# Performance work log

Hardware: AMD Instinct MI355X
Metric: run time of the kernel (lower is better)

Reference implementation:

```python
import jax, jax.numpy as jnp
import numpy as np

BOX = 32  # uniform ROI crop size (y1-y0 = x1-x0 = 32)


def setup_inputs() -> dict:
    key = jax.random.key(0)
    k1, k2, k3 = jax.random.split(key, 3)
    B, C, H, W = 8, 256, 200, 200
    N = 512
    feature_map = jax.random.normal(k1, (B, C, H, W), dtype=jnp.float32)
    boxes_yx = jax.random.randint(k2, (N, 2), 0, H - BOX, dtype=jnp.int32)  # top-left (y0, x0)
    assoc = jax.random.randint(k3, (N,), 0, B, dtype=jnp.int32)            # sample index per box
    return {"feature_map": feature_map, "boxes_yx": boxes_yx, "assoc": assoc}


def reference(feature_map, boxes_yx, assoc):
    # Faithful RoiCut: for each box i, crop feature_map[assoc[i], :, y0:y0+BOX, x0:x0+BOX].
    # clip_boxes=True -> clip box coords into the scene extent.
    B, C, H, W = feature_map.shape
    yx = jnp.clip(boxes_yx, 0, jnp.array([H - BOX, W - BOX], dtype=boxes_yx.dtype))

    def crop(a, yx_i):
        fm = feature_map[a]  # [C, H, W] gather of the associated sample
        return jax.lax.dynamic_slice(fm, (jnp.int32(0), yx_i[0], yx_i[1]), (C, BOX, BOX))

    box_features = jax.vmap(crop)(assoc, yx)  # [N, C, BOX, BOX]
    return box_features
```

## Files before the change

kernel.cpp:

```cpp
#include <hip/hip_runtime.h>


typedef float v4f __attribute__((ext_vector_type(4)));

constexpr int C_     = 256;
constexpr int H_     = 200;
constexpr int W_     = 200;
constexpr int BOX_   = 32;
constexpr int N_     = 512;
constexpr int B_     = 8;
constexpr int PLANE  = H_ * W_;
constexpr int HROWS  = 100;
constexpr int HLDS   = HROWS * W_;
constexpr int HLDS4  = HLDS / 4;

__global__ __launch_bounds__(512) void sort_boxes_kernel(
    const int* __restrict__ boxes,
    const int* __restrict__ assoc,
    unsigned int* __restrict__ keys,
    int* __restrict__ starts)
{
    __shared__ unsigned int key[N_];
    int t = threadIdx.x;

    int y0 = boxes[2 * t];
    int x0 = boxes[2 * t + 1];
    y0 = min(max(y0, 0), H_ - BOX_);
    x0 = min(max(x0, 0), W_ - BOX_);
    unsigned int a = (unsigned int)assoc[t];
    key[t] = (a << 25) | ((unsigned int)y0 << 17) | ((unsigned int)x0 << 9) | (unsigned int)t;
    __syncthreads();

    for (int k = 2; k <= N_; k <<= 1) {
        for (int j = k >> 1; j > 0; j >>= 1) {
            int ixj = t ^ j;
            if (ixj > t) {
                unsigned int va = key[t], vb = key[ixj];
                bool asc = ((t & k) == 0);
                if ((va > vb) == asc) { key[t] = vb; key[ixj] = va; }
            }
            __syncthreads();
        }
    }

    unsigned int v = key[t];
    keys[t] = v;
    int at = (int)(v >> 25);
    int ap = (t == 0) ? -1 : (int)(key[t - 1] >> 25);
    for (int aa = ap + 1; aa <= at; ++aa) starts[aa] = t;
    if (t == N_ - 1) for (int aa = at + 1; aa <= B_; ++aa) starts[aa] = N_;
}

__global__ __launch_bounds__(1024, 8) void roicut_kernel(
    const float* __restrict__ fm,
    const unsigned int* __restrict__ keys,
    const int* __restrict__ starts,
    float* __restrict__ out)
{
    extern __shared__ float lds[];

    int bid = blockIdx.x;
    int h = bid & 1;
    int c = (bid >> 1) & 255;
    int a = bid >> 9;
    int t = threadIdx.x;

    const v4f* src = (const v4f*)(fm + (size_t)(a * C_ + c) * PLANE) + h * HLDS4;
    v4f* l4 = (v4f*)lds;
    v4f r0 = src[t];
    v4f r1 = src[t + 1024];
    v4f r2 = src[t + 2048];
    v4f r3 = src[t + 3072];
    bool tail = t < (HLDS4 - 4096);
    v4f r4;
    if (tail) r4 = src[t + 4096];
    l4[t]        = r0;
    l4[t + 1024] = r1;
    l4[t + 2048] = r2;
    l4[t + 3072] = r3;
    if (tail) l4[t + 4096] = r4;
    __syncthreads();

    int b0 = starts[a], b1 = starts[a + 1];
    int sub = t >> 8;
    int q   = t & 255;
    int y   = q >> 3;
    int xg  = (q & 7) << 2;
    int hbase = h * HROWS;

    for (int b = b0; b < b1; b += 4) {
        int bb = b + sub;
        if (bb < b1) {
            unsigned int v = keys[bb];
            int y0 = (v >> 17) & 255;
            int x0 = (v >> 9) & 255;
            int i  = (int)(v & 511u);
            int ly = y0 + y - hbase;
            if (ly >= 0 && ly < HROWS) {
                const float* p = lds + ly * W_ + (x0 + xg);
                v4f vv;
                vv[0] = p[0];
                vv[1] = p[1];
                vv[2] = p[2];
                vv[3] = p[3];
                v4f* dst = (v4f*)(out + (((size_t)i << 18) + ((size_t)c << 10) + (size_t)(q << 2)));
                __builtin_nontemporal_store(vv, dst);
            }
        }
    }
}

extern "C" void kernel_launch(void* const* d_in, const int* in_sizes, int n_in,
                              void* d_out, int out_size, void* d_ws, size_t ws_size,
                              hipStream_t stream) {
    const float* fm    = (const float*)d_in[0];
    const int*   boxes = (const int*)d_in[1];
    const int*   assoc = (const int*)d_in[2];
    float*       out   = (float*)d_out;

    unsigned int* keys   = (unsigned int*)d_ws;
    int*          starts = (int*)d_ws + N_;

    (void)hipFuncSetAttribute((const void*)roicut_kernel,
                              hipFuncAttributeMaxDynamicSharedMemorySize,
                              HLDS * (int)sizeof(float));

    sort_boxes_kernel<<<1, N_, 0, stream>>>(boxes, assoc, keys, starts);

    int grid = B_ * C_ * 2;
    roicut_kernel<<<grid, 1024, HLDS * sizeof(float), stream>>>(fm, keys, starts, out);
}
```

Before: 172.5 us.

## Replace bitonic sort with atomic bucketing and software-pipeline the two half-plane loads

```diff
diff --git a/kernel.cpp b/kernel.cpp
--- a/kernel.cpp
+++ b/kernel.cpp
@@ -14,41 +14,36 @@
 constexpr int HLDS   = HROWS * W_;
 constexpr int HLDS4  = HLDS / 4;
 
-__global__ __launch_bounds__(512) void sort_boxes_kernel(
+__global__ __launch_bounds__(512) void group_boxes_kernel(
     const int* __restrict__ boxes,
     const int* __restrict__ assoc,
     unsigned int* __restrict__ keys,
     int* __restrict__ starts)
 {
-    __shared__ unsigned int key[N_];
+    __shared__ int cnt[B_];
+    __shared__ int base[B_ + 1];
     int t = threadIdx.x;
+
+    if (t < B_) cnt[t] = 0;
+    __syncthreads();
 
     int y0 = boxes[2 * t];
     int x0 = boxes[2 * t + 1];
     y0 = min(max(y0, 0), H_ - BOX_);
     x0 = min(max(x0, 0), W_ - BOX_);
-    unsigned int a = (unsigned int)assoc[t];
-    key[t] = (a << 25) | ((unsigned int)y0 << 17) | ((unsigned int)x0 << 9) | (unsigned int)t;
+    int a = assoc[t];
+    int pos = atomicAdd(&cnt[a], 1);
     __syncthreads();
 
-    for (int k = 2; k <= N_; k <<= 1) {
-        for (int j = k >> 1; j > 0; j >>= 1) {
-            int ixj = t ^ j;
-            if (ixj > t) {
-                unsigned int va = key[t], vb = key[ixj];
-                bool asc = ((t & k) == 0);
-                if ((va > vb) == asc) { key[t] = vb; key[ixj] = va; }
-            }
-            __syncthreads();
-        }
+    if (t == 0) {
+        int s = 0;
+        for (int i = 0; i < B_; ++i) { base[i] = s; s += cnt[i]; }
+        base[B_] = s;
     }
+    __syncthreads();
 
-    unsigned int v = key[t];
-    keys[t] = v;
-    int at = (int)(v >> 25);
-    int ap = (t == 0) ? -1 : (int)(key[t - 1] >> 25);
-    for (int aa = ap + 1; aa <= at; ++aa) starts[aa] = t;
-    if (t == N_ - 1) for (int aa = at + 1; aa <= B_; ++aa) starts[aa] = N_;
+    keys[base[a] + pos] = ((unsigned int)y0 << 17) | ((unsigned int)x0 << 9) | (unsigned int)t;
+    if (t <= B_) starts[t] = base[t];
 }
 
 __global__ __launch_bounds__(1024, 8) void roicut_kernel(
@@ -60,18 +55,24 @@
     extern __shared__ float lds[];
 
     int bid = blockIdx.x;
-    int h = bid & 1;
-    int c = (bid >> 1) & 255;
-    int a = bid >> 9;
+    int c = bid & 255;
+    int a = bid >> 8;
     int t = threadIdx.x;
 
-    const v4f* src = (const v4f*)(fm + (size_t)(a * C_ + c) * PLANE) + h * HLDS4;
+    int b0 = starts[a], b1 = starts[a + 1];
+    int sub = t >> 8;
+    int q   = t & 255;
+    int y   = q >> 3;
+    int xg  = (q & 7) << 2;
+
+    const v4f* src = (const v4f*)(fm + (size_t)(a * C_ + c) * PLANE);
     v4f* l4 = (v4f*)lds;
+    bool tail = t < (HLDS4 - 4096);
+
     v4f r0 = src[t];
     v4f r1 = src[t + 1024];
     v4f r2 = src[t + 2048];
     v4f r3 = src[t + 3072];
-    bool tail = t < (HLDS4 - 4096);
     v4f r4;
     if (tail) r4 = src[t + 4096];
     l4[t]        = r0;
@@ -81,30 +82,60 @@
     if (tail) l4[t + 4096] = r4;
     __syncthreads();
 
-    int b0 = starts[a], b1 = starts[a + 1];
-    int sub = t >> 8;
-    int q   = t & 255;
-    int y   = q >> 3;
-    int xg  = (q & 7) << 2;
-    int hbase = h * HROWS;
+    const v4f* src1 = src + HLDS4;
+    r0 = src1[t];
+    r1 = src1[t + 1024];
+    r2 = src1[t + 2048];
+    r3 = src1[t + 3072];
+    if (tail) r4 = src1[t + 4096];
+    __builtin_amdgcn_sched_barrier(0);
 
-    for (int b = b0; b < b1; b += 4) {
-        int bb = b + sub;
-        if (bb < b1) {
-            unsigned int v = keys[bb];
-            int y0 = (v >> 17) & 255;
-            int x0 = (v >> 9) & 255;
-            int i  = (int)(v & 511u);
-            int ly = y0 + y - hbase;
-            if (ly >= 0 && ly < HROWS) {
-                const float* p = lds + ly * W_ + (x0 + xg);
-                v4f vv;
-                vv[0] = p[0];
-                vv[1] = p[1];
-                vv[2] = p[2];
-                vv[3] = p[3];
-                v4f* dst = (v4f*)(out + (((size_t)i << 18) + ((size_t)c << 10) + (size_t)(q << 2)));
-                __builtin_nontemporal_store(vv, dst);
+    {
+        const int hbase = 0;
+        for (int b = b0; b < b1; b += 4) {
+            int bb = b + sub;
+            if (bb < b1) {
+                unsigned int v = keys[bb];
+                int y0 = (v >> 17) & 255;
+                int x0 = (v >> 9) & 255;
+                int i  = (int)(v & 511u);
+                int ly = y0 + y - hbase;
+                if (ly >= 0 && ly < HROWS) {
+                    const float* p = lds + ly * W_ + (x0 + xg);
+                    v4f vv;
+                    vv[0] = p[0]; vv[1] = p[1]; vv[2] = p[2]; vv[3] = p[3];
+                    v4f* dst = (v4f*)(out + (((size_t)i << 18) + ((size_t)c << 10) + (size_t)(q << 2)));
+                    __builtin_nontemporal_store(vv, dst);
+                }
+            }
+        }
+    }
+    __syncthreads();
+
+    l4[t]        = r0;
+    l4[t + 1024] = r1;
+    l4[t + 2048] = r2;
+    l4[t + 3072] = r3;
+    if (tail) l4[t + 4096] = r4;
+    __syncthreads();
+
+    {
+        const int hbase = HROWS;
+        for (int b = b0; b < b1; b += 4) {
+            int bb = b + sub;
+            if (bb < b1) {
+                unsigned int v = keys[bb];
+                int y0 = (v >> 17) & 255;
+                int x0 = (v >> 9) & 255;
+                int i  = (int)(v & 511u);
+                int ly = y0 + y - hbase;
+                if (ly >= 0 && ly < HROWS) {
+                    const float* p = lds + ly * W_ + (x0 + xg);
+                    v4f vv;
+                    vv[0] = p[0]; vv[1] = p[1]; vv[2] = p[2]; vv[3] = p[3];
+                    v4f* dst = (v4f*)(out + (((size_t)i << 18) + ((size_t)c << 10) + (size_t)(q << 2)));
+                    __builtin_nontemporal_store(vv, dst);
+                }
             }
         }
     }
@@ -125,8 +156,8 @@
                               hipFuncAttributeMaxDynamicSharedMemorySize,
                               HLDS * (int)sizeof(float));
 
-    sort_boxes_kernel<<<1, N_, 0, stream>>>(boxes, assoc, keys, starts);
+    group_boxes_kernel<<<1, N_, 0, stream>>>(boxes, assoc, keys, starts);
 
-    int grid = B_ * C_ * 2;
+    int grid = B_ * C_;
     roicut_kernel<<<grid, 1024, HLDS * sizeof(float), stream>>>(fm, keys, starts, out);
 }
```

New measurement: 176.8 us. +2.5%, slower.

## Split planes into quarter-row bands with binned box lists instead of sorted halves

Applied to the files above, without the earlier changes.

```diff
diff --git a/kernel.cpp b/kernel.cpp
--- a/kernel.cpp
+++ b/kernel.cpp
@@ -10,99 +10,107 @@
 constexpr int N_     = 512;
 constexpr int B_     = 8;
 constexpr int PLANE  = H_ * W_;
-constexpr int HROWS  = 100;
-constexpr int HLDS   = HROWS * W_;
-constexpr int HLDS4  = HLDS / 4;
+constexpr int QROWS  = 50;
+constexpr int NQ     = 4;
+constexpr int NBIN   = B_ * NQ;
+constexpr int QLDS   = QROWS * W_;
+constexpr int QLDS4  = QLDS / 4;
 
-__global__ __launch_bounds__(512) void sort_boxes_kernel(
+__global__ __launch_bounds__(512) void group_boxes_kernel(
     const int* __restrict__ boxes,
     const int* __restrict__ assoc,
     unsigned int* __restrict__ keys,
     int* __restrict__ starts)
 {
-    __shared__ unsigned int key[N_];
+    __shared__ int cnt[NBIN];
+    __shared__ int base[NBIN + 1];
     int t = threadIdx.x;
+
+    if (t < NBIN) cnt[t] = 0;
+    __syncthreads();
 
     int y0 = boxes[2 * t];
     int x0 = boxes[2 * t + 1];
     y0 = min(max(y0, 0), H_ - BOX_);
     x0 = min(max(x0, 0), W_ - BOX_);
-    unsigned int a = (unsigned int)assoc[t];
-    key[t] = (a << 25) | ((unsigned int)y0 << 17) | ((unsigned int)x0 << 9) | (unsigned int)t;
+    int a = assoc[t];
+    unsigned int key = ((unsigned int)y0 << 17) | ((unsigned int)x0 << 9) | (unsigned int)t;
+
+    int q0 = y0 / QROWS;
+    int q1 = (y0 + BOX_ - 1) / QROWS;
+    int bin0 = a * NQ + q0;
+    int p0 = atomicAdd(&cnt[bin0], 1);
+    int bin1 = -1, p1 = -1;
+    if (q1 != q0) {
+        bin1 = a * NQ + q1;
+        p1 = atomicAdd(&cnt[bin1], 1);
+    }
     __syncthreads();
 
-    for (int k = 2; k <= N_; k <<= 1) {
-        for (int j = k >> 1; j > 0; j >>= 1) {
-            int ixj = t ^ j;
-            if (ixj > t) {
-                unsigned int va = key[t], vb = key[ixj];
-                bool asc = ((t & k) == 0);
-                if ((va > vb) == asc) { key[t] = vb; key[ixj] = va; }
-            }
-            __syncthreads();
-        }
+    if (t == 0) {
+        int s = 0;
+        for (int i = 0; i < NBIN; ++i) { base[i] = s; s += cnt[i]; }
+        base[NBIN] = s;
     }
+    __syncthreads();
 
-    unsigned int v = key[t];
-    keys[t] = v;
-    int at = (int)(v >> 25);
-    int ap = (t == 0) ? -1 : (int)(key[t - 1] >> 25);
-    for (int aa = ap + 1; aa <= at; ++aa) starts[aa] = t;
-    if (t == N_ - 1) for (int aa = at + 1; aa <= B_; ++aa) starts[aa] = N_;
+    keys[base[bin0] + p0] = key;
+    if (p1 >= 0) keys[base[bin1] + p1] = key;
+    if (t <= NBIN) starts[t] = base[t];
 }
 
-__global__ __launch_bounds__(1024, 8) void roicut_kernel(
+__global__ __launch_bounds__(512, 8) void roicut_kernel(
     const float* __restrict__ fm,
     const unsigned int* __restrict__ keys,
     const int* __restrict__ starts,
     float* __restrict__ out)
 {
-    extern __shared__ float lds[];
+    __shared__ float lds[QLDS];
 
     int bid = blockIdx.x;
-    int h = bid & 1;
-    int c = (bid >> 1) & 255;
-    int a = bid >> 9;
-    int t = threadIdx.x;
+    int qtr = bid & 3;
+    int c   = (bid >> 2) & 255;
+    int a   = bid >> 10;
+    int t   = threadIdx.x;
 
-    const v4f* src = (const v4f*)(fm + (size_t)(a * C_ + c) * PLANE) + h * HLDS4;
+    int bin = a * NQ + qtr;
+    int b0 = starts[bin], b1 = starts[bin + 1];
+    if (b0 == b1) return;
+
+    const v4f* src = (const v4f*)(fm + (size_t)(a * C_ + c) * PLANE) + qtr * QLDS4;
     v4f* l4 = (v4f*)lds;
     v4f r0 = src[t];
-    v4f r1 = src[t + 1024];
-    v4f r2 = src[t + 2048];
-    v4f r3 = src[t + 3072];
-    bool tail = t < (HLDS4 - 4096);
+    v4f r1 = src[t + 512];
+    v4f r2 = src[t + 1024];
+    v4f r3 = src[t + 1536];
+    bool tail = t < (QLDS4 - 2048);
     v4f r4;
-    if (tail) r4 = src[t + 4096];
+    if (tail) r4 = src[t + 2048];
     l4[t]        = r0;
-    l4[t + 1024] = r1;
-    l4[t + 2048] = r2;
-    l4[t + 3072] = r3;
-    if (tail) l4[t + 4096] = r4;
+    l4[t + 512]  = r1;
+    l4[t + 1024] = r2;
+    l4[t + 1536] = r3;
+    if (tail) l4[t + 2048] = r4;
     __syncthreads();
 
-    int b0 = starts[a], b1 = starts[a + 1];
-    int sub = t >> 8;
-    int q   = t & 255;
-    int y   = q >> 3;
-    int xg  = (q & 7) << 2;
-    int hbase = h * HROWS;
+    int sub   = t >> 8;
+    int q     = t & 255;
+    int y     = q >> 3;
+    int xg    = (q & 7) << 2;
+    int rbase = qtr * QROWS;
 
-    for (int b = b0; b < b1; b += 4) {
+    for (int b = b0; b < b1; b += 2) {
         int bb = b + sub;
         if (bb < b1) {
             unsigned int v = keys[bb];
             int y0 = (v >> 17) & 255;
             int x0 = (v >> 9) & 255;
             int i  = (int)(v & 511u);
-            int ly = y0 + y - hbase;
-            if (ly >= 0 && ly < HROWS) {
+            int ly = y0 + y - rbase;
+            if (ly >= 0 && ly < QROWS) {
                 const float* p = lds + ly * W_ + (x0 + xg);
                 v4f vv;
-                vv[0] = p[0];
-                vv[1] = p[1];
-                vv[2] = p[2];
-                vv[3] = p[3];
+                vv[0] = p[0]; vv[1] = p[1]; vv[2] = p[2]; vv[3] = p[3];
                 v4f* dst = (v4f*)(out + (((size_t)i << 18) + ((size_t)c << 10) + (size_t)(q << 2)));
                 __builtin_nontemporal_store(vv, dst);
             }
@@ -119,14 +127,10 @@
     float*       out   = (float*)d_out;
 
     unsigned int* keys   = (unsigned int*)d_ws;
-    int*          starts = (int*)d_ws + N_;
+    int*          starts = (int*)d_ws + 2 * N_;
 
-    (void)hipFuncSetAttribute((const void*)roicut_kernel,
-                              hipFuncAttributeMaxDynamicSharedMemorySize,
-                              HLDS * (int)sizeof(float));
+    group_boxes_kernel<<<1, N_, 0, stream>>>(boxes, assoc, keys, starts);
 
-    sort_boxes_kernel<<<1, N_, 0, stream>>>(boxes, assoc, keys, starts);
-
-    int grid = B_ * C_ * 2;
-    roicut_kernel<<<grid, 1024, HLDS * sizeof(float), stream>>>(fm, keys, starts, out);
+    int grid = B_ * C_ * NQ;
+    roicut_kernel<<<grid, 512, 0, stream>>>(fm, keys, starts, out);
 }
```

New measurement: 180.6 us. 4.7% more time.
